# Performance work log

Measured on AMD Instinct MI355X. Metric: run time of the kernel, lower is better.

Reference implementation:

```python
import jax, jax.numpy as jnp
import numpy as np

NUM_LABELS = 64
START, END, PAD = 0, 1, 2
B, L, V, D = 128, 1024, 30000, 256


def make_transitions(key):
    # replicates CRF.init_weights
    t = jax.random.uniform(key, (NUM_LABELS, NUM_LABELS), minval=-0.1, maxval=0.1)
    t = t.at[:, START].set(-10000.0)
    t = t.at[END, :].set(-10000.0)
    t = t.at[PAD, :].set(-10000.0)
    t = t.at[:, PAD].set(-10000.0)
    t = t.at[PAD, PAD].set(0.0)
    t = t.at[PAD, END].set(0.0)
    return t.astype(jnp.float32)


def setup_inputs() -> dict:
    key = jax.random.key(0)
    k0, k1, k2, k3, k4 = jax.random.split(key, 5)
    x = jax.random.randint(k0, (B, L), 0, V)
    tags = jax.random.randint(k1, (B, L), 0, NUM_LABELS)
    mask = jnp.ones((B, L), dtype=jnp.float32)  # ignored by CRF (source passes mask=None)
    embed = jax.random.normal(k2, (V, D), dtype=jnp.float32)
    W = jax.random.normal(k3, (D, NUM_LABELS), dtype=jnp.float32) * 0.05
    b = jnp.zeros((NUM_LABELS,), dtype=jnp.float32)
    trans = make_transitions(k4)
    return {"x": x, "tags": tags, "mask": mask, "embed": embed, "W": W, "b": b, "trans": trans}


def _crf_nll(emissions, tags, trans):
    # emissions: [B, L, T]; tags: [B, L]; trans: [T, T]
    # NOTE: original CRF.forward ignores the user mask (passes mask=None ->
    # all-ones mask), so every position is valid and last tag is tags[:, -1].
    # gold path score
    e_scores = jnp.take_along_axis(emissions, tags[:, :, None], axis=2)[:, :, 0].sum(axis=1)
    t_scores = trans[tags[:, :-1], tags[:, 1:]].sum(axis=1)
    scores = e_scores + t_scores + trans[START, tags[:, 0]] + trans[tags[:, -1], END]
    # log partition: forward algorithm (log-space recursion over time)
    alpha0 = trans[START][None, :] + emissions[:, 0]  # [B, T]

    def step(alphas, emit_t):
        # alphas: [B, T_prev] -> logsumexp over previous tag
        new = jax.nn.logsumexp(alphas[:, :, None] + trans[None, :, :], axis=1) + emit_t
        return new, None

    alphas, _ = jax.lax.scan(step, alpha0, jnp.swapaxes(emissions[:, 1:], 0, 1))
    log_z = jax.nn.logsumexp(alphas + trans[:, END][None, :], axis=1)  # [B]
    return -jnp.sum(scores - log_z)


def reference(x, tags, mask, embed, W, b, trans):
    emissions = embed[x] @ W + b  # [B, L, T]
    return _crf_nll(emissions, tags, trans)
```

## Files before the change

kernel.cpp:

```cpp
#include <hip/hip_runtime.h>
#include <hip/hip_bf16.h>

#define B_ 128
#define L_ 1024
#define T_ 64
#define CSH 5
#define C_ 32

using short8 = __attribute__((ext_vector_type(8))) short;
using f32x4  = __attribute__((ext_vector_type(4))) float;
using f32x16 = __attribute__((ext_vector_type(16))) float;

static __device__ __forceinline__ unsigned short bfb(float x) {
  return __builtin_bit_cast(unsigned short, __float2bfloat16(x));
}
static __device__ __forceinline__ float asf(unsigned u) { return __builtin_bit_cast(float, u); }
static __device__ __forceinline__ unsigned pk2(float lo, float hi) {
  __hip_bfloat162 h = __float22bfloat162_rn(float2{lo, hi});
  unsigned u;
  __builtin_memcpy(&u, &h, 4);
  return u;
}
static __device__ __forceinline__ unsigned pk2t(float lo, float hi) {
  return __builtin_amdgcn_perm(__builtin_bit_cast(unsigned, hi),
                               __builtin_bit_cast(unsigned, lo), 0x07060302u);
}
static __device__ __forceinline__ void pswap(unsigned& x, unsigned& y) {
  asm("v_permlane32_swap_b32 %0, %1" : "+v"(x), "+v"(y));
}

__global__ __launch_bounds__(256) void k_prep(const float* __restrict__ W,
                                              unsigned short* __restrict__ Wswz,
                                              float* __restrict__ score,
                                              float* __restrict__ out) {
  if (blockIdx.x == 0) {
    if (threadIdx.x < 128) score[threadIdx.x] = 0.f;
    if (threadIdx.x == 0) out[0] = 0.f;
  }
  const int t = blockIdx.x * 256 + threadIdx.x;
  const int e = t * 4, k = e >> 6, n0 = e & 63;
  float4 w4 = *(const float4*)(W + e);
  const int base = ((k >> 5) << 11) + ((n0 >> 4) << 9) + (((k >> 3) & 3) << 7) +
                   ((n0 & 15) << 3) + (k & 7);
  Wswz[base + 0]  = bfb(w4.x);
  Wswz[base + 8]  = bfb(w4.y);
  Wswz[base + 16] = bfb(w4.z);
  Wswz[base + 24] = bfb(w4.w);
}

__global__ __launch_bounds__(256) void k_scan(const int* __restrict__ x,
                                              const int* __restrict__ tags,
                                              const float* __restrict__ embed,
                                              const unsigned short* __restrict__ Wswz,
                                              const float* __restrict__ bias,
                                              const float* __restrict__ trans,
                                              uint4* __restrict__ XT,
                                              float* __restrict__ rlog,
                                              float* __restrict__ score) {
  __shared__ __align__(16) float Ftile[4][2048];
  const int wv = threadIdx.x >> 6, L = threadIdx.x & 63;
  const int job = blockIdx.x * 4 + wv;
  const int c = job & (C_ - 1);
  const int b = job >> CSH;
  const int K = (1023 + C_ - 1) >> CSH;
  const int a = 1 + c * K;
  const int len = min(K, 1024 - a);
  const int nh = L & 31, hh = L >> 5;
  const int m = L & 15, q = L >> 4;
  float* Ft = Ftile[wv];
  const int* tg = tags + (size_t)b * L_;

  const float bj0 = bias[m], bj1 = bias[16 + m], bj2 = bias[32 + m], bj3 = bias[48 + m];
  for (int p = 0; p < 2; p++) {
    int tok = a + 16 * p + m;
    if (tok > 1023) tok = 1023;
    const float* er = embed + (size_t)x[b * 1024 + tok] * 256;
    f32x4 acc[4] = {{0.f,0.f,0.f,0.f},{0.f,0.f,0.f,0.f},{0.f,0.f,0.f,0.f},{0.f,0.f,0.f,0.f}};
#pragma unroll
    for (int kap = 0; kap < 8; kap++) {
      float4 p0 = *(const float4*)(er + 32 * kap + 8 * q);
      float4 p1 = *(const float4*)(er + 32 * kap + 8 * q + 4);
      unsigned u0 = pk2(p0.x, p0.y), u1 = pk2(p0.z, p0.w);
      unsigned u2 = pk2(p1.x, p1.y), u3 = pk2(p1.z, p1.w);
      short8 af = __builtin_bit_cast(short8, make_uint4(u0, u1, u2, u3));
#pragma unroll
      for (int u = 0; u < 4; u++) {
        short8 bf8 = *(const short8*)&Wswz[kap * 2048 + u * 512 + q * 128 + m * 8];
        acc[u] = __builtin_amdgcn_mfma_f32_16x16x32_bf16(af, bf8, acc[u], 0, 0, 0);
      }
    }
#pragma unroll
    for (int r = 0; r < 4; r++) {
      float e0 = acc[0][r] + bj0, e1 = acc[1][r] + bj1;
      float e2 = acc[2][r] + bj2, e3 = acc[3][r] + bj3;
      float mr = fmaxf(fmaxf(e0, e1), fmaxf(e2, e3));
#pragma unroll
      for (int off = 1; off < 16; off <<= 1) mr = fmaxf(mr, __shfl_xor(mr, off));
      float x0 = __expf(e0 - mr), x1 = __expf(e1 - mr);
      float x2 = __expf(e2 - mr), x3 = __expf(e3 - mr);
      float sr = (x0 + x1) + (x2 + x3);
#pragma unroll
      for (int off = 1; off < 16; off <<= 1) sr += __shfl_xor(sr, off);
      float rs = 1.0f / sr;
      const int row = 16 * p + 4 * q + r;
      Ft[row * 64 + m]      = x0 * rs;
      Ft[row * 64 + 16 + m] = x1 * rs;
      Ft[row * 64 + 32 + m] = x2 * rs;
      Ft[row * 64 + 48 + m] = x3 * rs;
    }
  }
  {
    float gold = 0.f;
    if (L < len) {
      const int tga = tg[a + L], tgp = tg[a - 1 + L];
      gold = __logf(Ft[L * 64 + tga]) + trans[tgp * T_ + tga];
    }
#pragma unroll
    for (int off = 1; off < 64; off <<= 1) gold += __shfl_xor(gold, off);
    if (L == 0) atomicAdd(&score[b], gold);
  }

  short8 Af[2][4];
#pragma unroll
  for (int I = 0; I < 2; I++)
#pragma unroll
    for (int kap = 0; kap < 4; kap++) {
      short8 aa;
#pragma unroll
      for (int d = 0; d < 8; d++) {
        const int k = 16 * kap + 8 * hh + d;
        aa[d] = (short)bfb(__expf(trans[k * T_ + 32 * I + nh]));
      }
      Af[I][kap] = aa;
    }
  unsigned Bf[4][2][4];
#pragma unroll
  for (int kap = 0; kap < 4; kap++)
#pragma unroll
    for (int J = 0; J < 2; J++)
#pragma unroll
      for (int dw = 0; dw < 4; dw++) {
        int k0 = 16 * kap + 8 * hh + 2 * dw, n = 32 * J + nh;
        unsigned u = 0;
        if (k0 == n) u = 0x3F80u;
        if (k0 + 1 == n) u = 0x3F800000u;
        Bf[kap][J][dw] = u;
      }

  float logacc = 0.f;
  const f32x16 Z = {};
  for (int s = 0; s < len; s++) {
    f32x16 Fv[2];
#pragma unroll
    for (int I = 0; I < 2; I++)
#pragma unroll
      for (int j = 0; j < 4; j++) {
        f32x4 f4 = *(const f32x4*)&Ft[s * 64 + 32 * I + 8 * j + 4 * hh];
#pragma unroll
        for (int e = 0; e < 4; e++) Fv[I][4 * j + e] = f4[e];
      }
    const bool rn = ((s & 15) == 15);
    float rs = 1.0f;
#pragma unroll
    for (int J = 0; J < 2; J++) {
      f32x16 D[2];
#pragma unroll
      for (int I = 0; I < 2; I++) {
        short8 b0 = __builtin_bit_cast(short8,
            make_uint4(Bf[0][J][0], Bf[0][J][1], Bf[0][J][2], Bf[0][J][3]));
        f32x16 d = __builtin_amdgcn_mfma_f32_32x32x16_bf16(Af[I][0], b0, Z, 0, 0, 0);
#pragma unroll
        for (int kap = 1; kap < 4; kap++) {
          short8 bk = __builtin_bit_cast(short8,
              make_uint4(Bf[kap][J][0], Bf[kap][J][1], Bf[kap][J][2], Bf[kap][J][3]));
          d = __builtin_amdgcn_mfma_f32_32x32x16_bf16(Af[I][kap], bk, d, 0, 0, 0);
        }
        D[I] = d;
      }
      D[0] *= Fv[0];
      D[1] *= Fv[1];
      if (rn) {
        if (J == 0) {
          float mx = D[0][0];
#pragma unroll
          for (int I = 0; I < 2; I++)
#pragma unroll
            for (int r = 0; r < 16; r++) mx = fmaxf(mx, D[I][r]);
#pragma unroll
          for (int off = 1; off < 64; off <<= 1) mx = fmaxf(mx, __shfl_xor(mx, off));
          rs = 1.0f / mx;
          logacc += __logf(mx);
        }
        D[0] *= rs;
        D[1] *= rs;
      }
      unsigned PDt[2][4][2];
#pragma unroll
      for (int I = 0; I < 2; I++)
#pragma unroll
        for (int j = 0; j < 4; j++) {
          PDt[I][j][0] = pk2t(D[I][4 * j + 0], D[I][4 * j + 1]);
          PDt[I][j][1] = pk2t(D[I][4 * j + 2], D[I][4 * j + 3]);
        }
#pragma unroll
      for (int kap = 0; kap < 4; kap++) {
        const int Ip = kap >> 1, e2 = 2 * (kap & 1);
        unsigned x0 = PDt[Ip][e2][0], y0 = PDt[Ip][e2 + 1][0];
        unsigned x1 = PDt[Ip][e2][1], y1 = PDt[Ip][e2 + 1][1];
        pswap(x0, y0);
        pswap(x1, y1);
        Bf[kap][J][0] = x0;
        Bf[kap][J][1] = x1;
        Bf[kap][J][2] = y0;
        Bf[kap][J][3] = y1;
      }
    }
  }
  {
    uint4* Xj = XT + (size_t)job * 512 + L;
#pragma unroll
    for (int J = 0; J < 2; J++)
#pragma unroll
      for (int kap = 0; kap < 4; kap++)
        Xj[(J * 4 + kap) * 64] =
            make_uint4(Bf[kap][J][0], Bf[kap][J][1], Bf[kap][J][2], Bf[kap][J][3]);
  }
  if (L == 0) rlog[job] = logacc;
}

__global__ __launch_bounds__(256) void k_tail(const uint4* __restrict__ XT,
                                              const float* __restrict__ rlog,
                                              const float* __restrict__ score,
                                              const int* __restrict__ x,
                                              const float* __restrict__ embed,
                                              const float* __restrict__ W,
                                              const float* __restrict__ bias,
                                              const float* __restrict__ trans,
                                              const int* __restrict__ tags,
                                              float* __restrict__ out) {
  __shared__ __align__(16) unsigned short Ptile[4][4096];
  __shared__ __align__(16) float vS[64];
  __shared__ float tlg[4];
  const int wv = threadIdx.x >> 6, L = threadIdx.x & 63;
  const int b = blockIdx.x;
  const int nh = L & 31, hh = L >> 5;
  const int* tg = tags + (size_t)b * L_;
  const f32x16 Z = {};
  unsigned Bf[4][2][4];

  const uint4* Sb4 = XT + ((size_t)(b * C_ + 8 * wv)) * 512 + L;
  {
    float plog = 0.f;
#pragma unroll
    for (int kap = 0; kap < 4; kap++)
#pragma unroll
      for (int J = 0; J < 2; J++)
#pragma unroll
        for (int dw = 0; dw < 4; dw++) {
          int k0 = 16 * kap + 8 * hh + 2 * dw, n = 32 * J + nh;
          unsigned u = 0;
          if (k0 == n) u = 0x3F80u;
          if (k0 + 1 == n) u = 0x3F800000u;
          Bf[kap][J][dw] = u;
        }
    uint4 Aq[2][4], Aqn[2][4];
#pragma unroll
    for (int I = 0; I < 2; I++)
#pragma unroll
      for (int kap = 0; kap < 4; kap++)
        Aq[I][kap] = Sb4[7 * 512 + (I * 4 + kap) * 64];
    for (int rr = 0; rr < 8; rr++) {
      const int r = 7 - rr;
      if (r > 0) {
#pragma unroll
        for (int I = 0; I < 2; I++)
#pragma unroll
          for (int kap = 0; kap < 4; kap++)
            Aqn[I][kap] = Sb4[(size_t)(r - 1) * 512 + (I * 4 + kap) * 64];
      }
      short8 Ap[2][4];
#pragma unroll
      for (int I = 0; I < 2; I++)
#pragma unroll
        for (int kap = 0; kap < 4; kap++)
          Ap[I][kap] = __builtin_bit_cast(short8, Aq[I][kap]);
      const bool last = (r == 0);
      float rsw = 1.0f;
#pragma unroll
      for (int J = 0; J < 2; J++) {
        f32x16 D[2];
#pragma unroll
        for (int I = 0; I < 2; I++) {
          short8 b0 = __builtin_bit_cast(short8,
              make_uint4(Bf[0][J][0], Bf[0][J][1], Bf[0][J][2], Bf[0][J][3]));
          f32x16 d = __builtin_amdgcn_mfma_f32_32x32x16_bf16(Ap[I][0], b0, Z, 0, 0, 0);
#pragma unroll
          for (int kap = 1; kap < 4; kap++) {
            short8 bk = __builtin_bit_cast(short8,
                make_uint4(Bf[kap][J][0], Bf[kap][J][1], Bf[kap][J][2], Bf[kap][J][3]));
            d = __builtin_amdgcn_mfma_f32_32x32x16_bf16(Ap[I][kap], bk, d, 0, 0, 0);
          }
          D[I] = d;
        }
        if (J == 0) {
          float mx = D[0][0];
#pragma unroll
          for (int I = 0; I < 2; I++)
#pragma unroll
            for (int rr2 = 0; rr2 < 16; rr2++) mx = fmaxf(mx, D[I][rr2]);
#pragma unroll
          for (int off = 1; off < 64; off <<= 1) mx = fmaxf(mx, __shfl_xor(mx, off));
          mx = fmaxf(mx, 1e-30f);
          rsw = 1.0f / mx;
          plog += __logf(mx);
        }
#pragma unroll
        for (int I = 0; I < 2; I++)
#pragma unroll
          for (int rr2 = 0; rr2 < 16; rr2++) D[I][rr2] *= rsw;
        unsigned PDt[2][4][2];
#pragma unroll
        for (int I = 0; I < 2; I++)
#pragma unroll
          for (int j = 0; j < 4; j++) {
            PDt[I][j][0] = pk2t(D[I][4 * j + 0], D[I][4 * j + 1]);
            PDt[I][j][1] = pk2t(D[I][4 * j + 2], D[I][4 * j + 3]);
          }
        if (last) {
          unsigned short* Xrow = Ptile[wv] + 32 * J + nh;
#pragma unroll
          for (int I = 0; I < 2; I++)
#pragma unroll
            for (int j = 0; j < 4; j++)
#pragma unroll
              for (int pp = 0; pp < 2; pp++) {
                const int rw = 32 * I + 8 * j + 4 * hh + 2 * pp;
                Xrow[rw * 64] = (unsigned short)(PDt[I][j][pp] & 0xffffu);
                Xrow[(rw + 1) * 64] = (unsigned short)(PDt[I][j][pp] >> 16);
              }
        } else {
#pragma unroll
          for (int kap = 0; kap < 4; kap++) {
            const int Ip = kap >> 1, e2 = 2 * (kap & 1);
            unsigned x0 = PDt[Ip][e2][0], y0 = PDt[Ip][e2 + 1][0];
            unsigned x1 = PDt[Ip][e2][1], y1 = PDt[Ip][e2 + 1][1];
            pswap(x0, y0);
            pswap(x1, y1);
            Bf[kap][J][0] = x0;
            Bf[kap][J][1] = x1;
            Bf[kap][J][2] = y0;
            Bf[kap][J][3] = y1;
          }
        }
      }
      if (r > 0) {
#pragma unroll
        for (int I = 0; I < 2; I++)
#pragma unroll
          for (int kap = 0; kap < 4; kap++)
            Aq[I][kap] = Aqn[I][kap];
      }
    }
    if (L == 0) tlg[wv] = plog;
  }
  __syncthreads();
  if (threadIdx.x >= 64) return;

  float tlog = (tlg[0] + tlg[1]) + (tlg[2] + tlg[3]);

  const int i = L;
  const float* er0 = embed + (size_t)x[(size_t)b * L_] * 256;
  float e0 = bias[i], e1 = 0.f, e2 = 0.f, e3 = 0.f;
#pragma unroll 16
  for (int d = 0; d < 256; d += 4) {
    e0 = fmaf(er0[d + 0], W[(d + 0) * T_ + i], e0);
    e1 = fmaf(er0[d + 1], W[(d + 1) * T_ + i], e1);
    e2 = fmaf(er0[d + 2], W[(d + 2) * T_ + i], e2);
    e3 = fmaf(er0[d + 3], W[(d + 3) * T_ + i], e3);
  }
  float e = (e0 + e1) + (e2 + e3);
  float mr = e;
#pragma unroll
  for (int off = 1; off < 64; off <<= 1) mr = fmaxf(mr, __shfl_xor(mr, off));
  float pex = __expf(e - mr);
  float sr = pex;
#pragma unroll
  for (int off = 1; off < 64; off <<= 1) sr += __shfl_xor(sr, off);
  const int t0 = tg[0];
  float sc = score[b];
  sc += (__shfl(e, t0) - mr) - __logf(sr);
  sc += trans[t0] + trans[tg[L_ - 1] * T_ + 1];
  vS[i] = __expf(trans[i]) * (pex / sr);
  float rl = (i < 32) ? rlog[b * C_ + i] : 0.f;
#pragma unroll
  for (int off = 1; off < 64; off <<= 1) rl += __shfl_xor(rl, off);

  float tacc = 0.f;
  {
#pragma unroll
    for (int kap = 0; kap < 4; kap++)
#pragma unroll
      for (int J = 0; J < 2; J++)
#pragma unroll
        for (int dw = 0; dw < 4; dw++) {
          int k0 = 16 * kap + 8 * hh + 2 * dw, n = 32 * J + nh;
          unsigned u = 0;
          if (k0 == n) u = 0x3F80u;
          if (k0 + 1 == n) u = 0x3F800000u;
          Bf[kap][J][dw] = u;
        }
    for (int rr = 0; rr < 4; rr++) {
      const int r = 3 - rr;
      short8 Ap[2][4];
#pragma unroll
      for (int I = 0; I < 2; I++)
#pragma unroll
        for (int kap = 0; kap < 4; kap++)
          Ap[I][kap] = *(const short8*)&Ptile[r][(32 * I + nh) * 64 + 16 * kap + 8 * hh];
      const bool last = (r == 0);
      float rsw = 1.0f;
#pragma unroll
      for (int J = 0; J < 2; J++) {
        f32x16 D[2];
#pragma unroll
        for (int I = 0; I < 2; I++) {
          short8 b0 = __builtin_bit_cast(short8,
              make_uint4(Bf[0][J][0], Bf[0][J][1], Bf[0][J][2], Bf[0][J][3]));
          f32x16 d = __builtin_amdgcn_mfma_f32_32x32x16_bf16(Ap[I][0], b0, Z, 0, 0, 0);
#pragma unroll
          for (int kap = 1; kap < 4; kap++) {
            short8 bk = __builtin_bit_cast(short8,
                make_uint4(Bf[kap][J][0], Bf[kap][J][1], Bf[kap][J][2], Bf[kap][J][3]));
            d = __builtin_amdgcn_mfma_f32_32x32x16_bf16(Ap[I][kap], bk, d, 0, 0, 0);
          }
          D[I] = d;
        }
        if (J == 0) {
          float mx = D[0][0];
#pragma unroll
          for (int I = 0; I < 2; I++)
#pragma unroll
            for (int rr2 = 0; rr2 < 16; rr2++) mx = fmaxf(mx, D[I][rr2]);
#pragma unroll
          for (int off = 1; off < 64; off <<= 1) mx = fmaxf(mx, __shfl_xor(mx, off));
          mx = fmaxf(mx, 1e-30f);
          rsw = 1.0f / mx;
          tlog += __logf(mx);
        }
#pragma unroll
        for (int I = 0; I < 2; I++)
#pragma unroll
          for (int rr2 = 0; rr2 < 16; rr2++) D[I][rr2] *= rsw;
        if (last) {
          float dJ = 0.f;
#pragma unroll
          for (int I = 0; I < 2; I++)
#pragma unroll
            for (int r2 = 0; r2 < 16; r2++)
              dJ = fmaf(D[I][r2], vS[32 * I + (r2 & 3) + 8 * (r2 >> 2) + 4 * hh], dJ);
          tacc = fmaf(__expf(trans[(32 * J + nh) * T_ + 1]), dJ, tacc);
        } else {
          unsigned PDt[2][4][2];
#pragma unroll
          for (int I = 0; I < 2; I++)
#pragma unroll
            for (int j = 0; j < 4; j++) {
              PDt[I][j][0] = pk2t(D[I][4 * j + 0], D[I][4 * j + 1]);
              PDt[I][j][1] = pk2t(D[I][4 * j + 2], D[I][4 * j + 3]);
            }
#pragma unroll
          for (int kap = 0; kap < 4; kap++) {
            const int Ip = kap >> 1, e2b = 2 * (kap & 1);
            unsigned x0 = PDt[Ip][e2b][0], y0 = PDt[Ip][e2b + 1][0];
            unsigned x1 = PDt[Ip][e2b][1], y1 = PDt[Ip][e2b + 1][1];
            pswap(x0, y0);
            pswap(x1, y1);
            Bf[kap][J][0] = x0;
            Bf[kap][J][1] = x1;
            Bf[kap][J][2] = y0;
            Bf[kap][J][3] = y1;
          }
        }
      }
    }
  }
  float t2 = tacc;
#pragma unroll
  for (int off = 1; off < 64; off <<= 1) t2 += __shfl_xor(t2, off);
  if (i == 0) {
    const float logz = rl + tlog + __logf(t2);
    atomicAdd(out, -(sc - logz));
  }
}

extern "C" void kernel_launch(void* const* d_in, const int* in_sizes, int n_in,
                              void* d_out, int out_size, void* d_ws, size_t ws_size,
                              hipStream_t stream) {
  const int* x = (const int*)d_in[0];
  const int* tags = (const int*)d_in[1];
  const float* embed = (const float*)d_in[3];
  const float* W = (const float*)d_in[4];
  const float* bias = (const float*)d_in[5];
  const float* trans = (const float*)d_in[6];

  char* ws = (char*)d_ws;
  uint4* XT = (uint4*)ws;
  float* rlog = (float*)(ws + (size_t)C_ * 1048576);
  float* score = (float*)((char*)rlog + 4096 * 4);
  unsigned short* Wswz = (unsigned short*)((char*)score + 128 * 4);
  float* out = (float*)d_out;

  k_prep<<<16, 256, 0, stream>>>(W, Wswz, score, out);
  k_scan<<<32 * C_, 256, 0, stream>>>(x, tags, embed, Wswz, bias, trans, XT, rlog, score);
  k_tail<<<B_, 256, 0, stream>>>(XT, rlog, score, x, embed, W, bias, trans, tags, out);
}
```

Measured before the change: 188.5 us.

## Split each scan chunk across four waves and combine sub-chunk products in LDS

Each block now handles one (batch, chunk) job rather than four. The 32-step chunk is split into four 8-step sub-chunks, one per wave. Waves 1-3 write their transfer-matrix products to shared memory, and wave 0 multiplies them together with renormalisation to form the chunk product. The aim is to shorten the serial MFMA dependency chain per wave by about four times. In exchange the block count rises fourfold, more shared memory and syncs are needed, and wave 0 does an extra serial combine of three matrix-matrix products.

```diff
diff --git a/kernel.cpp b/kernel.cpp
--- a/kernel.cpp
+++ b/kernel.cpp
@@ -6,6 +6,7 @@
 #define T_ 64
 #define CSH 5
 #define C_ 32
+#define ROWW 72
 
 using short8 = __attribute__((ext_vector_type(8))) short;
 using f32x4  = __attribute__((ext_vector_type(4))) float;
@@ -57,21 +58,23 @@
                                               uint4* __restrict__ XT,
                                               float* __restrict__ rlog,
                                               float* __restrict__ score) {
-  __shared__ __align__(16) float Ftile[4][2048];
+  __shared__ __align__(16) float Ftile[2048];
+  __shared__ __align__(16) unsigned short Pt[3][64 * ROWW];
+  __shared__ float chlog[4];
   const int wv = threadIdx.x >> 6, L = threadIdx.x & 63;
-  const int job = blockIdx.x * 4 + wv;
+  const int job = blockIdx.x;
   const int c = job & (C_ - 1);
   const int b = job >> CSH;
-  const int K = (1023 + C_ - 1) >> CSH;
-  const int a = 1 + c * K;
-  const int len = min(K, 1024 - a);
+  const int a = 1 + c * 32;
+  const int len = min(32, 1024 - a);
   const int nh = L & 31, hh = L >> 5;
   const int m = L & 15, q = L >> 4;
-  float* Ft = Ftile[wv];
+  float* Ft = Ftile;
   const int* tg = tags + (size_t)b * L_;
 
-  const float bj0 = bias[m], bj1 = bias[16 + m], bj2 = bias[32 + m], bj3 = bias[48 + m];
-  for (int p = 0; p < 2; p++) {
+  if (wv < 2) {
+    const float bj0 = bias[m], bj1 = bias[16 + m], bj2 = bias[32 + m], bj3 = bias[48 + m];
+    const int p = wv;
     int tok = a + 16 * p + m;
     if (tok > 1023) tok = 1023;
     const float* er = embed + (size_t)x[b * 1024 + tok] * 256;
@@ -109,7 +112,9 @@
       Ft[row * 64 + 48 + m] = x3 * rs;
     }
   }
-  {
+  __syncthreads();
+
+  if (wv == 0) {
     float gold = 0.f;
     if (L < len) {
       const int tga = tg[a + L], tgp = tg[a - 1 + L];
@@ -147,9 +152,11 @@
         Bf[kap][J][dw] = u;
       }
 
+  const int slo = 8 * wv;
+  const int send = min(slo + 8, len);
   float logacc = 0.f;
   const f32x16 Z = {};
-  for (int s = 0; s < len; s++) {
+  for (int s = slo; s < send; s++) {
     f32x16 Fv[2];
 #pragma unroll
     for (int I = 0; I < 2; I++)
@@ -159,7 +166,7 @@
 #pragma unroll
         for (int e = 0; e < 4; e++) Fv[I][4 * j + e] = f4[e];
       }
-    const bool rn = ((s & 15) == 15);
+    const bool last = (s == send - 1);
     float rs = 1.0f;
 #pragma unroll
     for (int J = 0; J < 2; J++) {
@@ -179,7 +186,7 @@
       }
       D[0] *= Fv[0];
       D[1] *= Fv[1];
-      if (rn) {
+      if (last) {
         if (J == 0) {
           float mx = D[0][0];
 #pragma unroll
@@ -194,6 +201,85 @@
         D[0] *= rs;
         D[1] *= rs;
       }
+      unsigned PDt[2][4][2];
+#pragma unroll
+      for (int I = 0; I < 2; I++)
+#pragma unroll
+        for (int j = 0; j < 4; j++) {
+          PDt[I][j][0] = pk2t(D[I][4 * j + 0], D[I][4 * j + 1]);
+          PDt[I][j][1] = pk2t(D[I][4 * j + 2], D[I][4 * j + 3]);
+        }
+      if (last && wv > 0) {
+        unsigned short* Xrow = Pt[wv - 1] + 32 * J + nh;
+#pragma unroll
+        for (int I = 0; I < 2; I++)
+#pragma unroll
+          for (int j = 0; j < 4; j++)
+#pragma unroll
+            for (int pp = 0; pp < 2; pp++) {
+              const int rw = 32 * I + 8 * j + 4 * hh + 2 * pp;
+              Xrow[rw * ROWW] = (unsigned short)(PDt[I][j][pp] & 0xffffu);
+              Xrow[(rw + 1) * ROWW] = (unsigned short)(PDt[I][j][pp] >> 16);
+            }
+      } else {
+#pragma unroll
+        for (int kap = 0; kap < 4; kap++) {
+          const int Ip = kap >> 1, e2 = 2 * (kap & 1);
+          unsigned x0 = PDt[Ip][e2][0], y0 = PDt[Ip][e2 + 1][0];
+          unsigned x1 = PDt[Ip][e2][1], y1 = PDt[Ip][e2 + 1][1];
+          pswap(x0, y0);
+          pswap(x1, y1);
+          Bf[kap][J][0] = x0;
+          Bf[kap][J][1] = x1;
+          Bf[kap][J][2] = y0;
+          Bf[kap][J][3] = y1;
+        }
+      }
+    }
+  }
+  if (L == 0) chlog[wv] = logacc;
+  __syncthreads();
+  if (wv != 0) return;
+
+  float clog = 0.f;
+  for (int w = 0; w < 3; w++) {
+    short8 Ap[2][4];
+#pragma unroll
+    for (int I = 0; I < 2; I++)
+#pragma unroll
+      for (int kap = 0; kap < 4; kap++)
+        Ap[I][kap] = *(const short8*)&Pt[w][(32 * I + nh) * ROWW + 16 * kap + 8 * hh];
+    float rsw = 1.0f;
+#pragma unroll
+    for (int J = 0; J < 2; J++) {
+      f32x16 D[2];
+#pragma unroll
+      for (int I = 0; I < 2; I++) {
+        short8 b0 = __builtin_bit_cast(short8,
+            make_uint4(Bf[0][J][0], Bf[0][J][1], Bf[0][J][2], Bf[0][J][3]));
+        f32x16 d = __builtin_amdgcn_mfma_f32_32x32x16_bf16(Ap[I][0], b0, Z, 0, 0, 0);
+#pragma unroll
+        for (int kap = 1; kap < 4; kap++) {
+          short8 bk = __builtin_bit_cast(short8,
+              make_uint4(Bf[kap][J][0], Bf[kap][J][1], Bf[kap][J][2], Bf[kap][J][3]));
+          d = __builtin_amdgcn_mfma_f32_32x32x16_bf16(Ap[I][kap], bk, d, 0, 0, 0);
+        }
+        D[I] = d;
+      }
+      if (J == 0) {
+        float mx = D[0][0];
+#pragma unroll
+        for (int I = 0; I < 2; I++)
+#pragma unroll
+          for (int r = 0; r < 16; r++) mx = fmaxf(mx, D[I][r]);
+#pragma unroll
+        for (int off = 1; off < 64; off <<= 1) mx = fmaxf(mx, __shfl_xor(mx, off));
+        mx = fmaxf(mx, 1e-30f);
+        rsw = 1.0f / mx;
+        clog += __logf(mx);
+      }
+      D[0] *= rsw;
+      D[1] *= rsw;
       unsigned PDt[2][4][2];
 #pragma unroll
       for (int I = 0; I < 2; I++)
@@ -225,7 +311,8 @@
         Xj[(J * 4 + kap) * 64] =
             make_uint4(Bf[kap][J][0], Bf[kap][J][1], Bf[kap][J][2], Bf[kap][J][3]);
   }
-  if (L == 0) rlog[job] = logacc;
+  if (L == 0)
+    rlog[job] = ((chlog[0] + chlog[1]) + (chlog[2] + chlog[3])) + clog;
 }
 
 __global__ __launch_bounds__(256) void k_tail(const uint4* __restrict__ XT,
@@ -511,6 +598,6 @@
   float* out = (float*)d_out;
 
   k_prep<<<16, 256, 0, stream>>>(W, Wswz, score, out);
-  k_scan<<<32 * C_, 256, 0, stream>>>(x, tags, embed, Wswz, bias, trans, XT, rlog, score);
+  k_scan<<<B_ * C_, 256, 0, stream>>>(x, tags, embed, Wswz, bias, trans, XT, rlog, score);
   k_tail<<<B_, 256, 0, stream>>>(XT, rlog, score, x, embed, W, bias, trans, tags, out);
 }
```

Result: slower. 277.5 us (+47.3%).

## Split emission computation from CRF scan into separate kernels with bf16 staging buffer

Applied to the files above, without the earlier changes.

The fused scan kernel, which computed emissions via MFMA and then ran the chunked forward recursion, becomes two kernels. k_emit computes normalized exp-emissions with two waves per job, one per 16-token half, and writes them to a global bf16 buffer. k_scan2 loads that buffer into LDS and runs the recursion, unpacking bf16 factors. This is meant to raise parallelism in the emission phase and halve LDS and register traffic for factors. The cost is an extra global round trip, an extra launch, and bf16 rounding of the emission factors. A two-pass fallback covers small workspaces.

```diff
diff --git a/kernel.cpp b/kernel.cpp
--- a/kernel.cpp
+++ b/kernel.cpp
@@ -48,30 +48,29 @@
   Wswz[base + 24] = bfb(w4.w);
 }
 
-__global__ __launch_bounds__(256) void k_scan(const int* __restrict__ x,
+__global__ __launch_bounds__(256) void k_emit(const int* __restrict__ x,
                                               const int* __restrict__ tags,
                                               const float* __restrict__ embed,
                                               const unsigned short* __restrict__ Wswz,
                                               const float* __restrict__ bias,
                                               const float* __restrict__ trans,
-                                              uint4* __restrict__ XT,
-                                              float* __restrict__ rlog,
-                                              float* __restrict__ score) {
-  __shared__ __align__(16) float Ftile[4][2048];
+                                              unsigned short* __restrict__ Fg,
+                                              float* __restrict__ score,
+                                              int job_base) {
+  __shared__ __align__(16) float Ftile[2][2048];
   const int wv = threadIdx.x >> 6, L = threadIdx.x & 63;
-  const int job = blockIdx.x * 4 + wv;
+  const int jl = wv >> 1, p = wv & 1;
+  const int job = job_base + blockIdx.x * 2 + jl;
   const int c = job & (C_ - 1);
   const int b = job >> CSH;
-  const int K = (1023 + C_ - 1) >> CSH;
-  const int a = 1 + c * K;
-  const int len = min(K, 1024 - a);
-  const int nh = L & 31, hh = L >> 5;
+  const int a = 1 + c * 32;
+  const int len = min(32, 1024 - a);
   const int m = L & 15, q = L >> 4;
-  float* Ft = Ftile[wv];
+  float* Ft = Ftile[jl];
   const int* tg = tags + (size_t)b * L_;
 
-  const float bj0 = bias[m], bj1 = bias[16 + m], bj2 = bias[32 + m], bj3 = bias[48 + m];
-  for (int p = 0; p < 2; p++) {
+  {
+    const float bj0 = bias[m], bj1 = bias[16 + m], bj2 = bias[32 + m], bj3 = bias[48 + m];
     int tok = a + 16 * p + m;
     if (tok > 1023) tok = 1023;
     const float* er = embed + (size_t)x[b * 1024 + tok] * 256;
@@ -109,7 +108,9 @@
       Ft[row * 64 + 48 + m] = x3 * rs;
     }
   }
-  {
+  __syncthreads();
+
+  if (p == 0) {
     float gold = 0.f;
     if (L < len) {
       const int tga = tg[a + L], tgp = tg[a - 1 + L];
@@ -118,6 +119,41 @@
 #pragma unroll
     for (int off = 1; off < 64; off <<= 1) gold += __shfl_xor(gold, off);
     if (L == 0) atomicAdd(&score[b], gold);
+  }
+
+  {
+    unsigned short* dst = Fg + (size_t)(job - job_base) * 2048 + p * 1024 + L * 16;
+    const float* src = Ft + p * 1024 + L * 16;
+    unsigned u[8];
+#pragma unroll
+    for (int k = 0; k < 8; k++)
+      u[k] = ((unsigned)bfb(src[2 * k + 1]) << 16) | (unsigned)bfb(src[2 * k]);
+    *(uint4*)dst = make_uint4(u[0], u[1], u[2], u[3]);
+    *(uint4*)(dst + 8) = make_uint4(u[4], u[5], u[6], u[7]);
+  }
+}
+
+__global__ __launch_bounds__(256) void k_scan2(const unsigned short* __restrict__ Fg,
+                                               const float* __restrict__ trans,
+                                               uint4* __restrict__ XT,
+                                               float* __restrict__ rlog,
+                                               int job_base) {
+  __shared__ __align__(16) unsigned short Ftile[4][2048];
+  const int wv = threadIdx.x >> 6, L = threadIdx.x & 63;
+  const int job = job_base + blockIdx.x * 4 + wv;
+  const int c = job & (C_ - 1);
+  const int a = 1 + c * 32;
+  const int len = min(32, 1024 - a);
+  const int nh = L & 31, hh = L >> 5;
+  unsigned short* Ft = Ftile[wv];
+
+  {
+    const uint4* src = (const uint4*)(Fg + (size_t)(job - job_base) * 2048);
+    uint4* dst = (uint4*)Ft;
+    dst[L] = src[L];
+    dst[64 + L] = src[64 + L];
+    dst[128 + L] = src[128 + L];
+    dst[192 + L] = src[192 + L];
   }
 
   short8 Af[2][4];
@@ -150,15 +186,12 @@
   float logacc = 0.f;
   const f32x16 Z = {};
   for (int s = 0; s < len; s++) {
-    f32x16 Fv[2];
+    uint2 Fc[2][4];
 #pragma unroll
     for (int I = 0; I < 2; I++)
 #pragma unroll
-      for (int j = 0; j < 4; j++) {
-        f32x4 f4 = *(const f32x4*)&Ft[s * 64 + 32 * I + 8 * j + 4 * hh];
-#pragma unroll
-        for (int e = 0; e < 4; e++) Fv[I][4 * j + e] = f4[e];
-      }
+      for (int j = 0; j < 4; j++)
+        Fc[I][j] = *(const uint2*)&Ft[s * 64 + (16 * I + 4 * j + 2 * hh) * 2];
     const bool rn = ((s & 15) == 15);
     float rs = 1.0f;
 #pragma unroll
@@ -177,8 +210,16 @@
         }
         D[I] = d;
       }
-      D[0] *= Fv[0];
-      D[1] *= Fv[1];
+#pragma unroll
+      for (int I = 0; I < 2; I++)
+#pragma unroll
+        for (int j = 0; j < 4; j++) {
+          uint2 g = Fc[I][j];
+          D[I][4 * j + 0] *= asf(g.x << 16);
+          D[I][4 * j + 1] *= asf(g.x & 0xffff0000u);
+          D[I][4 * j + 2] *= asf(g.y << 16);
+          D[I][4 * j + 3] *= asf(g.y & 0xffff0000u);
+        }
       if (rn) {
         if (J == 0) {
           float mx = D[0][0];
@@ -508,9 +549,21 @@
   float* rlog = (float*)(ws + (size_t)C_ * 1048576);
   float* score = (float*)((char*)rlog + 4096 * 4);
   unsigned short* Wswz = (unsigned short*)((char*)score + 128 * 4);
+  unsigned short* Fg = (unsigned short*)((char*)Wswz + 32768);
   float* out = (float*)d_out;
 
+  const size_t base_bytes = (size_t)C_ * 1048576 + 4096 * 4 + 128 * 4 + 32768;
+  const bool one_pass = ws_size >= base_bytes + (size_t)4096 * 2048 * 2;
+
   k_prep<<<16, 256, 0, stream>>>(W, Wswz, score, out);
-  k_scan<<<32 * C_, 256, 0, stream>>>(x, tags, embed, Wswz, bias, trans, XT, rlog, score);
+  if (one_pass) {
+    k_emit<<<2048, 256, 0, stream>>>(x, tags, embed, Wswz, bias, trans, Fg, score, 0);
+    k_scan2<<<1024, 256, 0, stream>>>(Fg, trans, XT, rlog, 0);
+  } else {
+    k_emit<<<1024, 256, 0, stream>>>(x, tags, embed, Wswz, bias, trans, Fg, score, 0);
+    k_scan2<<<512, 256, 0, stream>>>(Fg, trans, XT, rlog, 0);
+    k_emit<<<1024, 256, 0, stream>>>(x, tags, embed, Wswz, bias, trans, Fg, score, 2048);
+    k_scan2<<<512, 256, 0, stream>>>(Fg, trans, XT, rlog, 2048);
+  }
   k_tail<<<B_, 256, 0, stream>>>(XT, rlog, score, x, embed, W, bias, trans, tags, out);
 }
```

After: 207.5 us. 1.1x slower.
